# Kernel tuning notes

Hardware: AMD Instinct MI355X
Metric: run time of the kernel (lower is better)

The kernel has to match this reference:

```python
import jax, jax.numpy as jnp
import numpy as np

B, S, I, Q, H = 512, 196, 2048, 1024, 512


def _attn(X, g, wx, bx, wg, bg, wh, bh):
    # X: (B, S, F); g: (B, G) or None
    feat = jnp.einsum('bsf,fh->bsh', X, wx) + bx
    if g is not None:
        feat = feat + (g @ wg + bg)[:, None, :]
    h = jnp.tanh(feat)
    score = jnp.einsum('bsh,h->bs', h, wh) + bh  # (B, S)
    a = jax.nn.softmax(score, axis=1)
    return jnp.einsum('bs,bsf->bf', a, X)


def setup_inputs() -> dict:
    key = jax.random.key(0)
    ks = jax.random.split(key, 16)
    sc = lambda n: 1.0 / np.sqrt(n)
    d = {
        'ques_feat': jax.random.normal(ks[0], (B, Q), jnp.float32),
        'img_feat': jax.random.normal(ks[1], (B, S, I), jnp.float32),
        # attn1: X=ques (Q), no guidance
        'w1x': jax.random.uniform(ks[2], (Q, H), jnp.float32, -sc(Q), sc(Q)),
        'b1x': jnp.zeros((H,), jnp.float32),
        'w1h': jax.random.uniform(ks[3], (H,), jnp.float32, -sc(H), sc(H)),
        'b1h': jnp.zeros((), jnp.float32),
        # attn2: X=img (I), guidance=ques (Q)
        'w2x': jax.random.uniform(ks[4], (I, H), jnp.float32, -sc(I), sc(I)),
        'b2x': jnp.zeros((H,), jnp.float32),
        'w2g': jax.random.uniform(ks[5], (Q, H), jnp.float32, -sc(Q), sc(Q)),
        'b2g': jnp.zeros((H,), jnp.float32),
        'w2h': jax.random.uniform(ks[6], (H,), jnp.float32, -sc(H), sc(H)),
        'b2h': jnp.zeros((), jnp.float32),
        # attn3: X=ques (Q), guidance=img-attended (I)
        'w3x': jax.random.uniform(ks[7], (Q, H), jnp.float32, -sc(Q), sc(Q)),
        'b3x': jnp.zeros((H,), jnp.float32),
        'w3g': jax.random.uniform(ks[8], (I, H), jnp.float32, -sc(I), sc(I)),
        'b3g': jnp.zeros((H,), jnp.float32),
        'w3h': jax.random.uniform(ks[9], (H,), jnp.float32, -sc(H), sc(H)),
        'b3h': jnp.zeros((), jnp.float32),
    }
    return d


def reference(ques_feat, img_feat, w1x, b1x, w1h, b1h, w2x, b2x, w2g, b2g,
              w2h, b2h, w3x, b3x, w3g, b3g, w3h, b3h):
    q = ques_feat[:, None, :]  # (B, 1, Q)
    ques_self = _attn(q, None, w1x, b1x, None, None, w1h, b1h)          # (B, Q)
    img_attn = _attn(img_feat, ques_self, w2x, b2x, w2g, b2g, w2h, b2h)  # (B, I)
    ques_attn = _attn(q, img_attn, w3x, b3x, w3g, b3g, w3h, b3h)         # (B, Q)
    return (ques_attn, img_attn)
```

## Files before the change

### kernel.cpp

```cpp
#include <hip/hip_runtime.h>
#include <hip/hip_bf16.h>
#include <cstdint>


typedef __attribute__((ext_vector_type(8))) short bf16x8;
typedef __attribute__((ext_vector_type(4))) float f32x4;

typedef __attribute__((address_space(1))) const unsigned int as1_uint;
typedef __attribute__((address_space(3))) unsigned int as3_uint;

__device__ inline unsigned short f2bf(float f) {
    union { float f; unsigned u; } v; v.f = f;
    unsigned u = v.u;
    u += 0x7FFFu + ((u >> 16) & 1u);
    return (unsigned short)(u >> 16);
}

__device__ inline unsigned pk2(float lo, float hi) {
    __hip_bfloat162 h = __float22bfloat162_rn(make_float2(lo, hi));
    return *reinterpret_cast<unsigned*>(&h);
}

__device__ inline unsigned pkq(unsigned a, unsigned b) {
    union { unsigned u; float f; } x, y; x.u = a; y.u = b;
    return pk2(x.f, y.f);
}

__device__ inline bf16x8 cvt8(uint4 lo, uint4 hi) {
    union { unsigned u[4]; bf16x8 v; } r;
    r.u[0] = pkq(lo.x, lo.y); r.u[1] = pkq(lo.z, lo.w);
    r.u[2] = pkq(hi.x, hi.y); r.u[3] = pkq(hi.z, hi.w);
    return r.v;
}

__global__ void k_pack_w(const float* __restrict__ w, unsigned short* __restrict__ wtf) {
    int kblk = blockIdx.x >> 5;
    int nblk = blockIdx.x & 31;
    int t = threadIdx.x;
    int kc8 = t >> 4, col = t & 15;
    const float* src = w + (size_t)(kblk * 64 + kc8 * 8) * 512 + nblk * 16 + col;
    unsigned short* dst = wtf + (size_t)(kblk * 32 + nblk) * 1024 + kc8 * 128 + col * 8;
    unsigned short tmp[8];
    #pragma unroll
    for (int j = 0; j < 8; ++j) tmp[j] = f2bf(src[(size_t)j * 512]);
    *reinterpret_cast<uint4*>(dst) = *reinterpret_cast<const uint4*>(tmp);
}

__global__ void k_cconst(const float* __restrict__ qf, const float* __restrict__ w2g,
                         const float* __restrict__ b2g, const float* __restrict__ b2x,
                         float* __restrict__ cc, float* __restrict__ out0) {
    __shared__ float qls[2][1024];
    int b0 = blockIdx.x * 2;
    int t = threadIdx.x;
    #pragma unroll
    for (int j = 0; j < 2; ++j) {
        int idx = j * 256 + t;
        int bb = idx >> 8, c4 = idx & 255;
        float4 v = reinterpret_cast<const float4*>(qf + (size_t)(b0 + bb) * 1024)[c4];
        qls[bb][c4 * 4 + 0] = v.x; qls[bb][c4 * 4 + 1] = v.y;
        qls[bb][c4 * 4 + 2] = v.z; qls[bb][c4 * 4 + 3] = v.w;
        reinterpret_cast<float4*>(out0 + (size_t)(b0 + bb) * 1024)[c4] = v;
    }
    __syncthreads();
    float a00 = 0.f, a01 = 0.f, a10 = 0.f, a11 = 0.f;
    #pragma unroll 8
    for (int q = 0; q < 1024; ++q) {
        float w0 = w2g[q * 512 + t];
        float w1 = w2g[q * 512 + 256 + t];
        float q0 = qls[0][q], q1 = qls[1][q];
        a00 += q0 * w0; a01 += q0 * w1;
        a10 += q1 * w0; a11 += q1 * w1;
    }
    float c0 = b2g[t] + b2x[t];
    float c1 = b2g[t + 256] + b2x[t + 256];
    cc[(size_t)b0 * 512 + t] = a00 + c0;
    cc[(size_t)b0 * 512 + t + 256] = a01 + c1;
    cc[(size_t)(b0 + 1) * 512 + t] = a10 + c0;
    cc[(size_t)(b0 + 1) * 512 + t + 256] = a11 + c1;
}

#define NSTEP 32

__global__ __launch_bounds__(512, 4) void k_scores(
    const float* __restrict__ X, const unsigned short* __restrict__ WTf,
    const float* __restrict__ cc, const float* __restrict__ w2h,
    float* __restrict__ scores)
{
    __shared__ __align__(16) char Ab[4][16384];
    __shared__ __align__(16) char Bb[2][8192];
    __shared__ float slds[64];

    int tid = threadIdx.x;
    int wave = tid >> 6, lane = tid & 63;
    int l15 = lane & 15, l4 = lane >> 4;
    int r0 = blockIdx.x * 64;

    int srow = tid >> 4, spc = tid & 15;
    const char* xsrc = reinterpret_cast<const char*>(X + (size_t)(r0 + srow) * 2048)
                       + ((spc ^ (srow & 15)) << 4);
    const char* xsrc2 = xsrc + (size_t)32 * 8192;
    char* ldsw = &Ab[0][0] + wave * 1024;

    int cr = tid >> 3, co = tid & 7;
    int cvt_fL = cr * 256 + (((2 * co) ^ (cr & 15)) << 4);
    int cvt_fH = cr * 256 + (((2 * co + 1) ^ (cr & 15)) << 4);
    int cvt_w  = cr * 128 + ((co ^ (cr & 7)) << 4);

    const unsigned short* wb0 = WTf + (size_t)wave * 4096 + l4 * 128 + l15 * 8;

    const char* abase = &Ab[0][0];
    char* bbase = &Bb[0][0];
    int voffK0 = l15 * 128 + ((l4 ^ (l15 & 7)) << 4);
    int voffK1 = l15 * 128 + (((4 + l4) ^ (l15 & 7)) << 4);

    if (tid < 64) slds[tid] = 0.0f;

    f32x4 acc[4][4];
    #pragma unroll
    for (int m = 0; m < 4; ++m)
        #pragma unroll
        for (int n = 0; n < 4; ++n) acc[m][n] = (f32x4){0.f, 0.f, 0.f, 0.f};

    bf16x8 brA[4], brB[4];

    #define GLOAD2(bufofs, step) do { \
        __builtin_amdgcn_global_load_lds((as1_uint*)(xsrc + (step) * 256), \
            (as3_uint*)(ldsw + (bufofs)), 16, 0, 2); \
        __builtin_amdgcn_global_load_lds((as1_uint*)(xsrc2 + (step) * 256), \
            (as3_uint*)(ldsw + (bufofs) + 8192), 16, 0, 2); } while (0)

    #define BLOAD(dst, t, kh) do { \
        const unsigned short* bp = wb0 + (size_t)(t) * 32768 + (kh) * 512; \
        dst[0] = *reinterpret_cast<const bf16x8*>(bp); \
        dst[1] = *reinterpret_cast<const bf16x8*>(bp + 1024); \
        dst[2] = *reinterpret_cast<const bf16x8*>(bp + 2048); \
        dst[3] = *reinterpret_cast<const bf16x8*>(bp + 3072); } while (0)

    #define CONVERT(fbo, bbo) do { \
        uint4 lo = *reinterpret_cast<const uint4*>(abase + (fbo) + cvt_fL); \
        uint4 hi = *reinterpret_cast<const uint4*>(abase + (fbo) + cvt_fH); \
        *reinterpret_cast<bf16x8*>(bbase + (bbo) + cvt_w) = cvt8(lo, hi); } while (0)

    #define MF(br, bbo, voffK) do { \
        __builtin_amdgcn_s_setprio(1); \
        _Pragma("unroll") \
        for (int m = 0; m < 4; ++m) { \
            bf16x8 af = *reinterpret_cast<const bf16x8*>(bbase + (bbo) + m * 2048 + (voffK)); \
            _Pragma("unroll") \
            for (int n = 0; n < 4; ++n) \
                acc[m][n] = __builtin_amdgcn_mfma_f32_16x16x32_bf16(af, br[n], acc[m][n], 0, 0, 0); \
        } \
        __builtin_amdgcn_s_setprio(0); } while (0)

    #define SBAR __builtin_amdgcn_sched_barrier(0)

    GLOAD2(0, 0);
    GLOAD2(16384, 1);
    GLOAD2(32768, 2);
    BLOAD(brA, 0, 0);
    asm volatile("s_waitcnt vmcnt(8)" ::: "memory");
    CONVERT(0, 0);
    asm volatile("s_waitcnt lgkmcnt(0)" ::: "memory");
    __builtin_amdgcn_s_barrier();

    #pragma unroll 1
    for (int t = 0; t < NSTEP; ++t) {
        int bbo = (t & 1) * 8192;
        BLOAD(brB, t, 1);
        MF(brA, bbo, voffK0);
        if (t + 1 < NSTEP) BLOAD(brA, t + 1, 0);
        MF(brB, bbo, voffK1);
        if (t + 1 < NSTEP) CONVERT(((t + 1) & 3) * 16384, ((t + 1) & 1) * 8192);
        SBAR;
        if (t + 3 < NSTEP) GLOAD2(((t + 3) & 3) * 16384, t + 3);
        SBAR;
        asm volatile("s_waitcnt lgkmcnt(0)" ::: "memory");
        __builtin_amdgcn_s_barrier();
    }

    asm volatile("" ::: "memory");

    int b0 = r0 / 196;
    int sbreak = (b0 + 1) * 196 - r0;
    int b1 = b0 + 1; if (b1 > 511) b1 = 511;
    float cch0[4], cch1[4], whv[4];
    #pragma unroll
    for (int n = 0; n < 4; ++n) {
        int h = wave * 64 + n * 16 + l15;
        cch0[n] = cc[(size_t)b0 * 512 + h];
        cch1[n] = cc[(size_t)b1 * 512 + h];
        whv[n] = w2h[h];
    }
    #pragma unroll
    for (int m = 0; m < 4; ++m) {
        #pragma unroll
        for (int i = 0; i < 4; ++i) {
            int row = m * 16 + l4 * 4 + i;
            float p = 0.0f;
            #pragma unroll
            for (int n = 0; n < 4; ++n) {
                float x = acc[m][n][i] + ((row < sbreak) ? cch0[n] : cch1[n]);
                float th = 1.0f - 2.0f / (__expf(2.0f * x) + 1.0f);
                p += th * whv[n];
            }
            p += __shfl_xor(p, 1);
            p += __shfl_xor(p, 2);
            p += __shfl_xor(p, 4);
            p += __shfl_xor(p, 8);
            if (l15 == 0) atomicAdd(&slds[row], p);
        }
    }
    __syncthreads();
    if (tid < 64) scores[(size_t)r0 + tid] = slds[tid];
}

__global__ __launch_bounds__(256) void k_wsum_sm(const float* __restrict__ X,
                                                 const float* __restrict__ sc,
                                                 float* __restrict__ out1) {
    __shared__ float als[196];
    __shared__ float red[8];
    int b = blockIdx.x >> 1;
    int fh = (blockIdx.x & 1) * 1024;
    int t = threadIdx.x;

    float v = (t < 196) ? sc[(size_t)b * 196 + t] : -3.0e38f;
    float m = v;
    for (int o = 32; o > 0; o >>= 1) m = fmaxf(m, __shfl_xor(m, o));
    if ((t & 63) == 0) red[t >> 6] = m;
    __syncthreads();
    m = fmaxf(fmaxf(red[0], red[1]), fmaxf(red[2], red[3]));
    float e = (t < 196) ? __expf(v - m) : 0.0f;
    float s = e;
    for (int o = 32; o > 0; o >>= 1) s += __shfl_xor(s, o);
    if ((t & 63) == 0) red[4 + (t >> 6)] = s;
    __syncthreads();
    float tot = red[4] + red[5] + red[6] + red[7];
    if (t < 196) als[t] = e / tot;
    __syncthreads();

    int f = fh + t * 4;
    const float* Xb = X + (size_t)b * 196 * 2048 + f;
    float4 acc = {0.f, 0.f, 0.f, 0.f};
    #pragma unroll 4
    for (int ss = 0; ss < 196; ++ss) {
        float4 x = *reinterpret_cast<const float4*>(Xb + (size_t)ss * 2048);
        float w = als[ss];
        acc.x += w * x.x; acc.y += w * x.y; acc.z += w * x.z; acc.w += w * x.w;
    }
    *reinterpret_cast<float4*>(out1 + (size_t)b * 2048 + f) = acc;
}

extern "C" void kernel_launch(void* const* d_in, const int* in_sizes, int n_in,
                              void* d_out, int out_size, void* d_ws, size_t ws_size,
                              hipStream_t stream) {
    const float* qf  = (const float*)d_in[0];
    const float* X   = (const float*)d_in[1];
    const float* w2x = (const float*)d_in[6];
    const float* b2x = (const float*)d_in[7];
    const float* w2g = (const float*)d_in[8];
    const float* b2g = (const float*)d_in[9];
    const float* w2h = (const float*)d_in[10];

    float* out0 = (float*)d_out;
    float* out1 = out0 + 512 * 1024;

    unsigned short* WTf = (unsigned short*)d_ws;
    float* cc = (float*)((char*)d_ws + (size_t)(2u << 20));
    float* sc = (float*)((char*)d_ws + (size_t)(3u << 20));

    k_pack_w<<<1024, 128, 0, stream>>>(w2x, WTf);
    k_cconst<<<256, 256, 0, stream>>>(qf, w2g, b2g, b2x, cc, out0);
    k_scores<<<1568, 512, 0, stream>>>(X, WTf, cc, w2h, sc);
    k_wsum_sm<<<1024, 256, 0, stream>>>(X, sc, out1);
}
```

Before: 592.4 us.

## Shrink fp32 staging ring to three buffers and move conversion between MFMA halves

```diff
diff --git a/kernel.cpp b/kernel.cpp
--- a/kernel.cpp
+++ b/kernel.cpp
@@ -86,8 +86,8 @@
     const float* __restrict__ cc, const float* __restrict__ w2h,
     float* __restrict__ scores)
 {
-    __shared__ __align__(16) char Ab[4][16384];
-    __shared__ __align__(16) char Bb[2][8192];
+    __shared__ __align__(16) char Af[3][16384];
+    __shared__ __align__(16) char Bt[2][8192];
     __shared__ float slds[64];
 
     int tid = threadIdx.x;
@@ -99,18 +99,18 @@
     const char* xsrc = reinterpret_cast<const char*>(X + (size_t)(r0 + srow) * 2048)
                        + ((spc ^ (srow & 15)) << 4);
     const char* xsrc2 = xsrc + (size_t)32 * 8192;
-    char* ldsw = &Ab[0][0] + wave * 1024;
+    char* ldsw = &Af[0][0] + wave * 1024;
 
     int cr = tid >> 3, co = tid & 7;
     int cvt_fL = cr * 256 + (((2 * co) ^ (cr & 15)) << 4);
-    int cvt_fH = cr * 256 + (((2 * co + 1) ^ (cr & 15)) << 4);
+    int cvt_fH = cvt_fL ^ 16;
     int cvt_w  = cr * 128 + ((co ^ (cr & 7)) << 4);
 
     const unsigned short* wb0 = WTf + (size_t)wave * 4096 + l4 * 128 + l15 * 8;
 
-    const char* abase = &Ab[0][0];
-    char* bbase = &Bb[0][0];
-    int voffK0 = l15 * 128 + ((l4 ^ (l15 & 7)) << 4);
+    const char* fbase = &Af[0][0];
+    char* bbase = &Bt[0][0];
+    int voffK0 = l15 * 128 + (((0 + l4) ^ (l15 & 7)) << 4);
     int voffK1 = l15 * 128 + (((4 + l4) ^ (l15 & 7)) << 4);
 
     if (tid < 64) slds[tid] = 0.0f;
@@ -123,11 +123,11 @@
 
     bf16x8 brA[4], brB[4];
 
-    #define GLOAD2(bufofs, step) do { \
+    #define GLOAD2(fbo, step) do { \
         __builtin_amdgcn_global_load_lds((as1_uint*)(xsrc + (step) * 256), \
-            (as3_uint*)(ldsw + (bufofs)), 16, 0, 2); \
+            (as3_uint*)(ldsw + (fbo)), 16, 0, 2); \
         __builtin_amdgcn_global_load_lds((as1_uint*)(xsrc2 + (step) * 256), \
-            (as3_uint*)(ldsw + (bufofs) + 8192), 16, 0, 2); } while (0)
+            (as3_uint*)(ldsw + (fbo) + 8192), 16, 0, 2); } while (0)
 
     #define BLOAD(dst, t, kh) do { \
         const unsigned short* bp = wb0 + (size_t)(t) * 32768 + (kh) * 512; \
@@ -136,10 +136,10 @@
         dst[2] = *reinterpret_cast<const bf16x8*>(bp + 2048); \
         dst[3] = *reinterpret_cast<const bf16x8*>(bp + 3072); } while (0)
 
-    #define CONVERT(fbo, bbo) do { \
-        uint4 lo = *reinterpret_cast<const uint4*>(abase + (fbo) + cvt_fL); \
-        uint4 hi = *reinterpret_cast<const uint4*>(abase + (fbo) + cvt_fH); \
-        *reinterpret_cast<bf16x8*>(bbase + (bbo) + cvt_w) = cvt8(lo, hi); } while (0)
+    #define CONVERT(fbo, wbo) do { \
+        uint4 lo = *reinterpret_cast<const uint4*>(fbase + (fbo) + cvt_fL); \
+        uint4 hi = *reinterpret_cast<const uint4*>(fbase + (fbo) + cvt_fH); \
+        *reinterpret_cast<bf16x8*>(bbase + (wbo) + cvt_w) = cvt8(lo, hi); } while (0)
 
     #define MF(br, bbo, voffK) do { \
         __builtin_amdgcn_s_setprio(1); \
@@ -156,26 +156,34 @@
 
     GLOAD2(0, 0);
     GLOAD2(16384, 1);
-    GLOAD2(32768, 2);
     BLOAD(brA, 0, 0);
-    asm volatile("s_waitcnt vmcnt(8)" ::: "memory");
+    asm volatile("s_waitcnt vmcnt(6)" ::: "memory");
+    SBAR;
     CONVERT(0, 0);
     asm volatile("s_waitcnt lgkmcnt(0)" ::: "memory");
     __builtin_amdgcn_s_barrier();
 
+    int fcvt = 16384;
+    int fdma = 32768;
     #pragma unroll 1
     for (int t = 0; t < NSTEP; ++t) {
         int bbo = (t & 1) * 8192;
         BLOAD(brB, t, 1);
         MF(brA, bbo, voffK0);
-        if (t + 1 < NSTEP) BLOAD(brA, t + 1, 0);
+        if (t + 1 < NSTEP) {
+            asm volatile("s_waitcnt vmcnt(4)" ::: "memory");
+            SBAR;
+            CONVERT(fcvt, ((t + 1) & 1) * 8192);
+            BLOAD(brA, t + 1, 0);
+        }
         MF(brB, bbo, voffK1);
-        if (t + 1 < NSTEP) CONVERT(((t + 1) & 3) * 16384, ((t + 1) & 1) * 8192);
         SBAR;
-        if (t + 3 < NSTEP) GLOAD2(((t + 3) & 3) * 16384, t + 3);
+        if (t + 2 < NSTEP) GLOAD2(fdma, t + 2);
         SBAR;
         asm volatile("s_waitcnt lgkmcnt(0)" ::: "memory");
         __builtin_amdgcn_s_barrier();
+        fcvt = fdma;
+        fdma += 16384; if (fdma == 49152) fdma = 0;
     }
 
     asm volatile("" ::: "memory");
```

Result: faster. 491.0 us (-17.1%).
